# Kernel tuning notes

Measured on AMD Instinct MI355X. Metric: run time of the kernel, lower is better.

Reference implementation:

```python
import jax, jax.numpy as jnp
import numpy as np

N_NODES = 100000
N_EDGES = 1600000
IN_DIM, HID_DIM, N_CLS = 500, 64, 16


def spline_conv(x, edge_index, edge_attr, w, root, bias):
    """SplineConv with dim=1, kernel_size=2, degree=1, aggr='add'.

    For K=2, m=1 open B-spline: v = pseudo * (K - m) = pseudo in [0,1],
    basis = [(1 - v), v] with kernel indices [0, 1].
    """
    v = jnp.clip(edge_attr[:, 0], 0.0, 1.0 - 1e-6)  # [E]
    src, dst = edge_index[0], edge_index[1]
    # Precompute per-node transforms for both kernel indices (dense GEMMs),
    # then gather per-edge instead of gathering [in,out] weight matrices.
    xw0 = x @ w[0]  # [N, out]
    xw1 = x @ w[1]  # [N, out]
    msg = (1.0 - v)[:, None] * xw0[src] + v[:, None] * xw1[src]  # [E, out]
    agg = jax.ops.segment_sum(msg, dst, num_segments=x.shape[0])  # [N, out]
    return agg + x @ root + bias


def setup_inputs() -> dict:
    key = jax.random.key(0)
    ks = jax.random.split(key, 8)
    x = jax.random.normal(ks[0], (N_NODES, IN_DIM), dtype=jnp.float32)
    edge_index = jax.random.randint(ks[1], (2, N_EDGES), 0, N_NODES, dtype=jnp.int32)
    edge_attr = jax.random.uniform(ks[2], (N_EDGES, 1), dtype=jnp.float32)
    s1 = 1.0 / np.sqrt(IN_DIM)
    s2 = 1.0 / np.sqrt(HID_DIM)
    w1 = jax.random.normal(ks[3], (2, IN_DIM, HID_DIM), dtype=jnp.float32) * s1
    root1 = jax.random.normal(ks[4], (IN_DIM, HID_DIM), dtype=jnp.float32) * s1
    b1 = jnp.zeros((HID_DIM,), dtype=jnp.float32)
    w2 = jax.random.normal(ks[5], (2, HID_DIM, N_CLS), dtype=jnp.float32) * s2
    root2 = jax.random.normal(ks[6], (HID_DIM, N_CLS), dtype=jnp.float32) * s2
    b2 = jnp.zeros((N_CLS,), dtype=jnp.float32)
    return {"x": x, "edge_index": edge_index, "edge_attr": edge_attr,
            "w1": w1, "root1": root1, "b1": b1,
            "w2": w2, "root2": root2, "b2": b2}


def reference(x, edge_index, edge_attr, w1, root1, b1, w2, root2, b2):
    # dropout is identity at inference time
    h = spline_conv(x, edge_index, edge_attr, w1, root1, b1)
    h = jax.nn.relu(h)
    h = spline_conv(h, edge_index, edge_attr, w2, root2, b2)
    return jax.nn.log_softmax(h, axis=1)
```

## Files before the change

### kernel.cpp

```cpp
#include <hip/hip_runtime.h>
#include <math.h>

#define N_NODES 100000
#define N_EDGES 1600000
#define IN_DIM 500
#define HID 64
#define NCLS 16
#define KP 512
#define NSTEPS 16
#define NBUK 391
#define NPAD (NBUK * 256)
#define EPB_B 4096
#define NBB ((N_EDGES + EPB_B - 1) / EPB_B)
#define CAP 8192

typedef __attribute__((ext_vector_type(8))) short short8;
typedef __attribute__((ext_vector_type(4))) float f32x4;

__device__ __forceinline__ unsigned short f2bf(float f) {
    unsigned u = __builtin_bit_cast(unsigned, f);
    return (unsigned short)((u + 0x7FFFu + ((u >> 16) & 1u)) >> 16);
}
__device__ __forceinline__ float bf2f(unsigned short s) {
    unsigned u = ((unsigned)s) << 16;
    return __builtin_bit_cast(float, u);
}
__device__ __forceinline__ unsigned pack2(unsigned short a, unsigned short b) {
    return (unsigned)a | ((unsigned)b << 16);
}
__device__ __forceinline__ void gload16(const void* g, void* l) {
    __builtin_amdgcn_global_load_lds(
        (const __attribute__((address_space(1))) unsigned*)g,
        (__attribute__((address_space(3))) unsigned*)l, 16, 0, 0);
}

__global__ __launch_bounds__(256) void k0_bt(
    const float* __restrict__ w1, const float* __restrict__ root1,
    unsigned short* __restrict__ Bt, int* __restrict__ bkcur)
{
    const int b = blockIdx.x;
    if (b == 192) {
        for (int i = threadIdx.x; i < NBUK; i += 256) bkcur[i] = i * CAP;
        return;
    }
    const float* src;
    int c;
    if (b < 64)        { src = w1;                c = b; }
    else if (b < 128)  { src = w1 + IN_DIM * HID; c = b - 64; }
    else               { src = root1;             c = b - 128; }
    for (int k = threadIdx.x; k < KP; k += 256) {
        float v = (k < IN_DIM) ? src[k * HID + c] : 0.f;
        Bt[b * KP + k] = f2bf(v);
    }
}

union K1Smem {
    struct { float A[4][64 * 32]; unsigned short B[4][192 * 32]; } s;
    unsigned short O[64 * 264];
    struct { int hcnt[NBUK]; int hbase[NBUK]; } bk;
};

__global__ __launch_bounds__(256) void fat_bucket_k1(
    const int* __restrict__ ei, const float* __restrict__ ea,
    int* __restrict__ bkcur, uint2* __restrict__ epk,
    const float* __restrict__ x, const unsigned short* __restrict__ Bt,
    unsigned short* __restrict__ xw01, float* __restrict__ aggH)
{
    __shared__ K1Smem sm;
    const int tid = threadIdx.x;
    const int bi = blockIdx.x;

    if (bi % 5 == 0) {
        const int start = (bi / 5) * EPB_B;
        const int eend = min(start + EPB_B, N_EDGES);

        for (int i = tid; i < NBUK; i += 256) sm.bk.hcnt[i] = 0;
        __syncthreads();

#pragma unroll
        for (int j = 0; j < EPB_B / 256; ++j) {
            const int e = start + j * 256 + tid;
            if (e < eend) atomicAdd(&sm.bk.hcnt[ei[N_EDGES + e] >> 8], 1);
        }
        __syncthreads();

        for (int b = tid; b < NBUK; b += 256) {
            const int c = sm.bk.hcnt[b];
            sm.bk.hbase[b] = c ? atomicAdd(&bkcur[b], c) : 0;
        }
        __syncthreads();
        for (int i = tid; i < NBUK; i += 256) sm.bk.hcnt[i] = 0;
        __syncthreads();

#pragma unroll
        for (int j = 0; j < EPB_B / 256; ++j) {
            const int e = start + j * 256 + tid;
            if (e < eend) {
                const int src = ei[e];
                const int dst = ei[N_EDGES + e];
                const float v = fminf(fmaxf(ea[e], 0.f), 1.f - 1e-6f);
                const unsigned vq = (unsigned)(v * 16777216.0f);
                const int bk = dst >> 8;
                const int r = atomicAdd(&sm.bk.hcnt[bk], 1);
                epk[sm.bk.hbase[bk] + r] =
                    make_uint2((unsigned)src, ((unsigned)(dst & 255) << 24) | vq);
            }
        }
        return;
    }

    const int row0 = (bi - (bi + 4) / 5) * 64;
    const int w = tid >> 6;
    const int l = tid & 63;
    const int l16 = l & 15;
    const int koct = l >> 4;
    const int wr = w >> 1;
    const int wc = w & 1;

    f32x4 acc[2][6];
#pragma unroll
    for (int i = 0; i < 2; ++i)
#pragma unroll
        for (int j = 0; j < 6; ++j) acc[i][j] = (f32x4){0.f, 0.f, 0.f, 0.f};

    const int aChunk4 = (l & 7) * 4;
    const float* aBase[2];
    int aLdsOff[2];
#pragma unroll
    for (int i = 0; i < 2; ++i) {
        const int rowl = (2 * w + i) * 8 + (l >> 3);
        int grow = row0 + rowl;
        if (grow > N_NODES - 1) grow = N_NODES - 1;
        aBase[i] = x + (size_t)grow * IN_DIM;
        aLdsOff[i] = (2 * w + i) * 256;
    }
    const unsigned short* bBase[3];
    int bLdsOff[3];
#pragma unroll
    for (int i = 0; i < 3; ++i) {
        const int coll = (3 * w + i) * 16 + (l >> 2);
        bBase[i] = Bt + (size_t)coll * KP + (l & 3) * 8;
        bLdsOff[i] = (3 * w + i) * 512;
    }

    auto ISSUE = [&](int s) {
        const int k0 = s * 32;
        const int buf = s & 3;
#pragma unroll
        for (int i = 0; i < 2; ++i) {
            int gk = k0 + aChunk4; if (gk > IN_DIM - 4) gk = IN_DIM - 4;
            gload16(aBase[i] + gk, &sm.s.A[buf][aLdsOff[i]]);
        }
#pragma unroll
        for (int i = 0; i < 3; ++i)
            gload16(bBase[i] + k0, &sm.s.B[buf][bLdsOff[i]]);
    };

    ISSUE(0);
    ISSUE(1);
    ISSUE(2);

#pragma unroll
    for (int s = 0; s < NSTEPS; ++s) {
        if (s < NSTEPS - 2)       asm volatile("s_waitcnt vmcnt(10)" ::: "memory");
        else if (s == NSTEPS - 2) asm volatile("s_waitcnt vmcnt(5)" ::: "memory");
        else                      asm volatile("s_waitcnt vmcnt(0)" ::: "memory");
        __builtin_amdgcn_s_barrier();
        asm volatile("" ::: "memory");
        if (s + 3 < NSTEPS) ISSUE(s + 3);

        const int buf = s & 3;
        const float* LA = sm.s.A[buf];
        const unsigned short* LB = sm.s.B[buf];
        short8 af[2];
#pragma unroll
        for (int rb = 0; rb < 2; ++rb) {
            const int r = wr * 32 + rb * 16 + l16;
            f32x4 f0 = *(const f32x4*)&LA[r * 32 + koct * 8];
            f32x4 f1 = *(const f32x4*)&LA[r * 32 + koct * 8 + 4];
            short8 a;
            a[0] = (short)f2bf(f0[0]); a[1] = (short)f2bf(f0[1]);
            a[2] = (short)f2bf(f0[2]); a[3] = (short)f2bf(f0[3]);
            a[4] = (short)f2bf(f1[0]); a[5] = (short)f2bf(f1[1]);
            a[6] = (short)f2bf(f1[2]); a[7] = (short)f2bf(f1[3]);
            af[rb] = a;
        }
#pragma unroll
        for (int cf = 0; cf < 6; ++cf) {
            const int c = wc * 96 + cf * 16 + l16;
            short8 bfg = *(const short8*)&LB[c * 32 + koct * 8];
            acc[0][cf] = __builtin_amdgcn_mfma_f32_16x16x32_bf16(af[0], bfg, acc[0][cf], 0, 0, 0);
            acc[1][cf] = __builtin_amdgcn_mfma_f32_16x16x32_bf16(af[1], bfg, acc[1][cf], 0, 0, 0);
        }
    }
    __syncthreads();

#pragma unroll
    for (int rb = 0; rb < 2; ++rb)
#pragma unroll
        for (int cf = 0; cf < 6; ++cf) {
            const int cg = wc * 96 + cf * 16 + l16;
            if (96 * wc + cf * 16 < 128) {
#pragma unroll
                for (int reg = 0; reg < 4; ++reg) {
                    const int rloc = wr * 32 + rb * 16 + koct * 4 + reg;
                    const int idx = (cg < 64) ? (2 * cg) : (2 * cg - 127);
                    sm.O[rloc * 264 + idx] = f2bf(acc[rb][cf][reg]);
                }
            } else {
#pragma unroll
                for (int reg = 0; reg < 4; ++reg) {
                    const int r = row0 + wr * 32 + rb * 16 + koct * 4 + reg;
                    if (r < N_NODES) aggH[(size_t)r * HID + (cg - 128)] = acc[rb][cf][reg];
                }
            }
        }
    __syncthreads();
    {
        const int row = tid >> 2, q = tid & 3;
        const int rg = row0 + row;
        if (rg < N_NODES) {
#pragma unroll
            for (int j = 0; j < 4; ++j) {
                uint4 v = *(const uint4*)&sm.O[row * 264 + q * 32 + j * 8];
                *(uint4*)&xw01[(size_t)rg * 128 + q * 32 + j * 8] = v;
            }
        }
    }
}

__global__ __launch_bounds__(1024) void place_agg1(
    const int* __restrict__ bkcur, const uint2* __restrict__ epk,
    uint2* __restrict__ epkS, int* __restrict__ off, int* __restrict__ deg,
    const unsigned* __restrict__ xw01_u, float* __restrict__ aggH)
{
    __shared__ uint2 buf[CAP];
    __shared__ int hist[256];
    __shared__ int sc[256];
    __shared__ int cur[256];
    __shared__ int locs[256];
    __shared__ int degs[256];

    const int b = blockIdx.x;
    const int tid = threadIdx.x;
    const int start = b * CAP;
    const int cnt = bkcur[b] - start;

    if (tid < 256) hist[tid] = 0;
    __syncthreads();
    for (int i = tid; i < cnt; i += 1024)
        atomicAdd(&hist[epk[start + i].y >> 24], 1);
    __syncthreads();

    int val = 0;
    if (tid < 256) { val = hist[tid]; sc[tid] = val; }
    __syncthreads();
    for (int d = 1; d < 256; d <<= 1) {
        int add = 0;
        if (tid < 256 && tid >= d) add = sc[tid - d];
        __syncthreads();
        if (tid < 256) sc[tid] += add;
        __syncthreads();
    }
    if (tid < 256) {
        const int myloc = sc[tid] - val;
        off[(b << 8) + tid] = start + myloc;
        deg[(b << 8) + tid] = val;
        locs[tid] = myloc;
        degs[tid] = val;
        cur[tid] = myloc;
    }
    __syncthreads();

    for (int i = tid; i < cnt; i += 1024) {
        const uint2 u = epk[start + i];
        const int dl = u.y >> 24;
        const float v = (float)(u.y & 0xFFFFFFu) * 5.9604644775390625e-8f;
        const int pos = atomicAdd(&cur[dl], 1);
        buf[pos] = make_uint2(u.x, __builtin_bit_cast(unsigned, v));
    }
    __syncthreads();

    for (int i = tid; i < cnt; i += 1024)
        epkS[start + i] = buf[i];

    const int wv = tid >> 6;
    const int l = tid & 63;
#pragma unroll
    for (int t = 0; t < 16; ++t) {
        const int nl = wv * 16 + t;
        const int n = (b << 8) + nl;
        if (n >= N_NODES) continue;
        const int lst = locs[nl];
        const int dgn = degs[nl];

        float acc = aggH[(size_t)n * HID + l];
        for (int i = 0; i < dgn; i += 8) {
            unsigned srcs[8];
            float w0[8], w1[8];
#pragma unroll
            for (int j = 0; j < 8; ++j) {
                const bool ok = (i + j) < dgn;
                const int idx = lst + (ok ? i + j : 0);
                const uint2 u = buf[idx];
                const float v = __builtin_bit_cast(float, u.y);
                srcs[j] = u.x;
                w0[j] = ok ? (1.f - v) : 0.f;
                w1[j] = ok ? v : 0.f;
            }
            unsigned g[8];
#pragma unroll
            for (int j = 0; j < 8; ++j) g[j] = xw01_u[(size_t)srcs[j] * 64 + l];
#pragma unroll
            for (int j = 0; j < 8; ++j) {
                acc += w0[j] * bf2f((unsigned short)(g[j] & 0xFFFF));
                acc += w1[j] * bf2f((unsigned short)(g[j] >> 16));
            }
        }
        aggH[(size_t)n * HID + l] = acc;
    }
}

__global__ __launch_bounds__(256) void k3_relu_gemm(
    const float* __restrict__ aggH, const float* __restrict__ b1,
    const float* __restrict__ w2, const float* __restrict__ root2,
    unsigned* __restrict__ hw01_u, float* __restrict__ agg2)
{
    __shared__ float Ws[3 * HID * NCLS];
    __shared__ float Hs[16][HID];

    const int tid = threadIdx.x;
    for (int i = tid; i < 2 * HID * NCLS; i += 256) Ws[i] = w2[i];
    for (int i = tid; i < HID * NCLS; i += 256) Ws[2 * HID * NCLS + i] = root2[i];

    const int n0 = blockIdx.x * 16;
    for (int i = tid; i < 16 * HID; i += 256) {
        const int nl = i >> 6, k = i & 63;
        const float h = aggH[(size_t)(n0 + nl) * HID + k] + b1[k];
        Hs[nl][k] = fmaxf(h, 0.f);
    }
    __syncthreads();

    const int nl = tid >> 4;
    const int c = tid & 15;
    float a0 = 0.f, a1 = 0.f, a2 = 0.f;
#pragma unroll
    for (int k = 0; k < HID; ++k) {
        const float h = Hs[nl][k];
        a0 += h * Ws[0 * HID * NCLS + k * NCLS + c];
        a1 += h * Ws[1 * HID * NCLS + k * NCLS + c];
        a2 += h * Ws[2 * HID * NCLS + k * NCLS + c];
    }
    const size_t o = (size_t)(n0 + nl) * NCLS + c;
    hw01_u[o] = pack2(f2bf(a0), f2bf(a1));
    agg2[o] = a2;
}

__global__ __launch_bounds__(256) void agg2_sm(
    const int* __restrict__ off, const int* __restrict__ deg,
    const uint2* __restrict__ epk, const unsigned* __restrict__ hw01_u,
    const float* __restrict__ agg2, const float* __restrict__ b2,
    float* __restrict__ out)
{
    const int n = blockIdx.x * 16 + (threadIdx.x >> 4);
    const int c = threadIdx.x & 15;
    const int start = off[n];
    const int dg = deg[n];

    float acc = agg2[(size_t)n * NCLS + c];
    for (int i = 0; i < dg; i += 8) {
        unsigned srcs[8];
        float w0[8], w1[8];
#pragma unroll
        for (int j = 0; j < 8; ++j) {
            const bool ok = (i + j) < dg;
            const int idx = ok ? (start + i + j) : start;
            const uint2 t = epk[idx];
            const float v = __builtin_bit_cast(float, t.y);
            srcs[j] = t.x;
            w0[j] = ok ? (1.f - v) : 0.f;
            w1[j] = ok ? v : 0.f;
        }
        unsigned g[8];
#pragma unroll
        for (int j = 0; j < 8; ++j) g[j] = hw01_u[(size_t)srcs[j] * NCLS + c];
#pragma unroll
        for (int j = 0; j < 8; ++j) {
            acc += w0[j] * bf2f((unsigned short)(g[j] & 0xFFFF));
            acc += w1[j] * bf2f((unsigned short)(g[j] >> 16));
        }
    }

    const float z = acc + b2[c];
    float m = z;
#pragma unroll
    for (int s = 1; s < 16; s <<= 1) m = fmaxf(m, __shfl_xor(m, s, 64));
    const float e = expf(z - m);
    float ssum = e;
#pragma unroll
    for (int s = 1; s < 16; s <<= 1) ssum += __shfl_xor(ssum, s, 64);
    out[(size_t)n * NCLS + c] = (z - m) - logf(ssum);
}

extern "C" void kernel_launch(void* const* d_in, const int* in_sizes, int n_in,
                              void* d_out, int out_size, void* d_ws, size_t ws_size,
                              hipStream_t stream) {
    const float* x = (const float*)d_in[0];
    const int* ei = (const int*)d_in[1];
    const float* ea = (const float*)d_in[2];
    const float* w1 = (const float*)d_in[3];
    const float* root1 = (const float*)d_in[4];
    const float* b1 = (const float*)d_in[5];
    const float* w2 = (const float*)d_in[6];
    const float* root2 = (const float*)d_in[7];
    const float* b2 = (const float*)d_in[8];
    float* out = (float*)d_out;

    char* ws = (char*)d_ws;
    unsigned short* xw01 = (unsigned short*)ws;
    float* aggH = (float*)(ws + 25600000);
    unsigned* hw01_u = (unsigned*)(ws + 51200000);
    float* agg2 = (float*)(ws + 57600000);
    unsigned short* Bt = (unsigned short*)(ws + 64000000);
    int* off = (int*)(ws + 64300000);
    int* deg = (int*)(ws + 64800000);
    int* bkcur = (int*)(ws + 65300000);
    uint2* epk = (uint2*)(ws + 65400000);
    uint2* epkS = (uint2*)(ws + 91100000);

    k0_bt<<<193, 256, 0, stream>>>(w1, root1, Bt, bkcur);

    fat_bucket_k1<<<NBB + (N_NODES + 63) / 64, 256, 0, stream>>>(
        ei, ea, bkcur, epk, x, Bt, xw01, aggH);

    place_agg1<<<NBUK, 1024, 0, stream>>>(bkcur, epk, epkS, off, deg,
                                          (const unsigned*)xw01, aggH);
    k3_relu_gemm<<<N_NODES / 16, 256, 0, stream>>>(aggH, b1, w2, root2, hw01_u, agg2);
    agg2_sm<<<N_NODES / 16, 256, 0, stream>>>(off, deg, epkS, hw01_u, agg2, b2, out);
}
```

Baseline: 244.0 us.

## Fuse layer-1 aggregation with ReLU and layer-2 GEMM using bf16 MFMA

Merges the k3_relu_gemm kernel into the bucketed layer-1 aggregation kernel. The aggregated hidden rows stay in registers, are bias-added and ReLU'd into LDS as bf16, and are multiplied by the transposed w2/root2 with MFMA 16x16x32 bf16. This removes one kernel launch and the write and re-read of the 64-wide aggH buffer. It adds LDS use and register pressure in a 1024-thread block, and rounds the second-layer inputs and weights to bf16.

```diff
diff --git a/kernel.cpp b/kernel.cpp
--- a/kernel.cpp
+++ b/kernel.cpp
@@ -13,6 +13,7 @@
 #define EPB_B 4096
 #define NBB ((N_EDGES + EPB_B - 1) / EPB_B)
 #define CAP 8192
+#define HP 72
 
 typedef __attribute__((ext_vector_type(8))) short short8;
 typedef __attribute__((ext_vector_type(4))) float f32x4;
@@ -229,12 +230,16 @@
     }
 }
 
-__global__ __launch_bounds__(1024) void place_agg1(
+__global__ __launch_bounds__(1024) void place_agg1_k3(
     const int* __restrict__ bkcur, const uint2* __restrict__ epk,
     uint2* __restrict__ epkS, int* __restrict__ off, int* __restrict__ deg,
-    const unsigned* __restrict__ xw01_u, float* __restrict__ aggH)
+    const unsigned* __restrict__ xw01_u, const float* __restrict__ aggH,
+    const float* __restrict__ b1, const float* __restrict__ w2,
+    const float* __restrict__ root2, unsigned* __restrict__ hw01_u,
+    float* __restrict__ agg2)
 {
     __shared__ uint2 buf[CAP];
+    __shared__ unsigned short W2t[48 * HP];
     __shared__ int hist[256];
     __shared__ int sc[256];
     __shared__ int cur[256];
@@ -245,6 +250,15 @@
     const int tid = threadIdx.x;
     const int start = b * CAP;
     const int cnt = bkcur[b] - start;
+
+    for (int i = tid; i < 48 * 64; i += 1024) {
+        const int col = i >> 6, k = i & 63;
+        float v;
+        if (col < 16)      v = w2[k * NCLS + col];
+        else if (col < 32) v = w2[HID * NCLS + k * NCLS + (col - 16)];
+        else               v = root2[k * NCLS + (col - 32)];
+        W2t[col * HP + k] = f2bf(v);
+    }
 
     if (tid < 256) hist[tid] = 0;
     __syncthreads();
@@ -286,74 +300,75 @@
 
     const int wv = tid >> 6;
     const int l = tid & 63;
+    const float b1v = b1[l];
+    float acct[16];
 #pragma unroll
     for (int t = 0; t < 16; ++t) {
         const int nl = wv * 16 + t;
         const int n = (b << 8) + nl;
-        if (n >= N_NODES) continue;
-        const int lst = locs[nl];
-        const int dgn = degs[nl];
-
-        float acc = aggH[(size_t)n * HID + l];
-        for (int i = 0; i < dgn; i += 8) {
-            unsigned srcs[8];
-            float w0[8], w1[8];
-#pragma unroll
-            for (int j = 0; j < 8; ++j) {
-                const bool ok = (i + j) < dgn;
-                const int idx = lst + (ok ? i + j : 0);
-                const uint2 u = buf[idx];
-                const float v = __builtin_bit_cast(float, u.y);
-                srcs[j] = u.x;
-                w0[j] = ok ? (1.f - v) : 0.f;
-                w1[j] = ok ? v : 0.f;
+        float acc = 0.f;
+        if (n < N_NODES) {
+            const int lst = locs[nl];
+            const int dgn = degs[nl];
+            acc = aggH[(size_t)n * HID + l];
+            for (int i = 0; i < dgn; i += 8) {
+                unsigned srcs[8];
+                float w0[8], w1v[8];
+#pragma unroll
+                for (int j = 0; j < 8; ++j) {
+                    const bool ok = (i + j) < dgn;
+                    const int idx = lst + (ok ? i + j : 0);
+                    const uint2 u = buf[idx];
+                    const float v = __builtin_bit_cast(float, u.y);
+                    srcs[j] = u.x;
+                    w0[j] = ok ? (1.f - v) : 0.f;
+                    w1v[j] = ok ? v : 0.f;
+                }
+                unsigned g[8];
+#pragma unroll
+                for (int j = 0; j < 8; ++j) g[j] = xw01_u[(size_t)srcs[j] * 64 + l];
+#pragma unroll
+                for (int j = 0; j < 8; ++j) {
+                    acc += w0[j] * bf2f((unsigned short)(g[j] & 0xFFFF));
+                    acc += w1v[j] * bf2f((unsigned short)(g[j] >> 16));
+                }
             }
-            unsigned g[8];
-#pragma unroll
-            for (int j = 0; j < 8; ++j) g[j] = xw01_u[(size_t)srcs[j] * 64 + l];
-#pragma unroll
-            for (int j = 0; j < 8; ++j) {
-                acc += w0[j] * bf2f((unsigned short)(g[j] & 0xFFFF));
-                acc += w1[j] * bf2f((unsigned short)(g[j] >> 16));
-            }
-        }
-        aggH[(size_t)n * HID + l] = acc;
-    }
-}
-
-__global__ __launch_bounds__(256) void k3_relu_gemm(
-    const float* __restrict__ aggH, const float* __restrict__ b1,
-    const float* __restrict__ w2, const float* __restrict__ root2,
-    unsigned* __restrict__ hw01_u, float* __restrict__ agg2)
-{
-    __shared__ float Ws[3 * HID * NCLS];
-    __shared__ float Hs[16][HID];
-
-    const int tid = threadIdx.x;
-    for (int i = tid; i < 2 * HID * NCLS; i += 256) Ws[i] = w2[i];
-    for (int i = tid; i < HID * NCLS; i += 256) Ws[2 * HID * NCLS + i] = root2[i];
-
-    const int n0 = blockIdx.x * 16;
-    for (int i = tid; i < 16 * HID; i += 256) {
-        const int nl = i >> 6, k = i & 63;
-        const float h = aggH[(size_t)(n0 + nl) * HID + k] + b1[k];
-        Hs[nl][k] = fmaxf(h, 0.f);
-    }
-    __syncthreads();
-
-    const int nl = tid >> 4;
-    const int c = tid & 15;
-    float a0 = 0.f, a1 = 0.f, a2 = 0.f;
-#pragma unroll
-    for (int k = 0; k < HID; ++k) {
-        const float h = Hs[nl][k];
-        a0 += h * Ws[0 * HID * NCLS + k * NCLS + c];
-        a1 += h * Ws[1 * HID * NCLS + k * NCLS + c];
-        a2 += h * Ws[2 * HID * NCLS + k * NCLS + c];
-    }
-    const size_t o = (size_t)(n0 + nl) * NCLS + c;
-    hw01_u[o] = pack2(f2bf(a0), f2bf(a1));
-    agg2[o] = a2;
+        }
+        acct[t] = acc;
+    }
+    __syncthreads();
+
+    unsigned short* hb = (unsigned short*)buf;
+#pragma unroll
+    for (int t = 0; t < 16; ++t) {
+        const int nl = wv * 16 + t;
+        hb[nl * HP + l] = f2bf(fmaxf(acct[t] + b1v, 0.f));
+    }
+    __syncthreads();
+
+    const int l16 = l & 15;
+    const int koct = l >> 4;
+    f32x4 c3[3];
+#pragma unroll
+    for (int j = 0; j < 3; ++j) c3[j] = (f32x4){0.f, 0.f, 0.f, 0.f};
+#pragma unroll
+    for (int s2 = 0; s2 < 2; ++s2) {
+        short8 a = *(const short8*)&hb[(wv * 16 + l16) * HP + s2 * 32 + koct * 8];
+#pragma unroll
+        for (int cf = 0; cf < 3; ++cf) {
+            short8 bf = *(const short8*)&W2t[(cf * 16 + l16) * HP + s2 * 32 + koct * 8];
+            c3[cf] = __builtin_amdgcn_mfma_f32_16x16x32_bf16(a, bf, c3[cf], 0, 0, 0);
+        }
+    }
+#pragma unroll
+    for (int reg = 0; reg < 4; ++reg) {
+        const int n = (b << 8) + wv * 16 + koct * 4 + reg;
+        if (n < N_NODES) {
+            hw01_u[(size_t)n * NCLS + l16] =
+                pack2(f2bf(c3[0][reg]), f2bf(c3[1][reg]));
+            agg2[(size_t)n * NCLS + l16] = c3[2][reg];
+        }
+    }
 }
 
 __global__ __launch_bounds__(256) void agg2_sm(
@@ -433,8 +448,8 @@
     fat_bucket_k1<<<NBB + (N_NODES + 63) / 64, 256, 0, stream>>>(
         ei, ea, bkcur, epk, x, Bt, xw01, aggH);
 
-    place_agg1<<<NBUK, 1024, 0, stream>>>(bkcur, epk, epkS, off, deg,
-                                          (const unsigned*)xw01, aggH);
-    k3_relu_gemm<<<N_NODES / 16, 256, 0, stream>>>(aggH, b1, w2, root2, hw01_u, agg2);
+    place_agg1_k3<<<NBUK, 1024, 0, stream>>>(bkcur, epk, epkS, off, deg,
+                                             (const unsigned*)xw01, aggH,
+                                             b1, w2, root2, hw01_u, agg2);
     agg2_sm<<<N_NODES / 16, 256, 0, stream>>>(off, deg, epkS, hw01_u, agg2, b2, out);
 }
```

New measurement: 214.1 us (median of 2 runs). -12.3%, faster.
